# Performance work log

Measured on AMD Instinct MI355X. Metric: run time of the kernel, lower is better.

## Reference

```python
import jax, jax.numpy as jnp
import numpy as np

B = 8192        # number of contexts
T_SIDE = 10     # num_cx_tokens_per_side
NT = 10         # cx_max_num_types
V_TOK = 5000
V_TYP = 5000
D_TOK = 128
D_TYP = 32
H = 32          # hole_rnn_layer_size
D_IN = D_TOK + D_TYP  # 160


def setup_inputs() -> dict:
    key = jax.random.key(0)
    ks = jax.random.split(key, 32)
    def n(k, shape, scale=1.0):
        return jax.random.normal(k, shape, dtype=jnp.float32) * scale
    def rmask(k, shape):
        m = jax.random.randint(k, shape, 0, 2).astype(bool)
        return m.at[:, :, 0].set(True)  # first type slot always valid (as in data loader)
    inp = {}
    inp['tokens_before'] = jax.random.randint(ks[0], (B, T_SIDE), 0, V_TOK, dtype=jnp.int32)
    inp['types_before'] = jax.random.randint(ks[1], (B, T_SIDE, NT), 0, V_TYP, dtype=jnp.int32)
    inp['mask_before'] = rmask(ks[2], (B, T_SIDE, NT))
    inp['tokens_after'] = jax.random.randint(ks[3], (B, T_SIDE), 0, V_TOK, dtype=jnp.int32)
    inp['types_after'] = jax.random.randint(ks[4], (B, T_SIDE, NT), 0, V_TYP, dtype=jnp.int32)
    inp['mask_after'] = rmask(ks[5], (B, T_SIDE, NT))
    inp['token_embeddings'] = n(ks[6], (V_TOK, D_TOK))
    inp['type_embeddings'] = n(ks[7], (V_TYP, D_TYP))
    inp['hole_representation'] = n(ks[8], (1, 1, D_IN))
    # GRU kernels (TF GRUCell layout): gate kernel [(in+h), 2h], candidate [(in+h), h]
    i = 9
    for layer, din in ((0, D_IN), (1, 2 * H)):
        for d in ('fw', 'bw'):
            inp[f'gk_{d}{layer}'] = n(ks[i], (din + H, 2 * H), 0.1); i += 1
            inp[f'gb_{d}{layer}'] = jnp.zeros((2 * H,), jnp.float32)
            inp[f'ck_{d}{layer}'] = n(ks[i], (din + H, H), 0.1); i += 1
            inp[f'cb_{d}{layer}'] = jnp.zeros((H,), jnp.float32)
    return inp


def _embed(tokens, types, mask, tok_emb, typ_emb):
    te = tok_emb[tokens]                                 # [B,T,128]
    ty = typ_emb[types]                                  # [B,T,NT,32]
    ty = ty + (1.0 - mask[..., None].astype(jnp.float32)) * -1000.0
    ty = jnp.max(ty, axis=2)                             # masked max over types -> [B,T,32]
    return jnp.concatenate([te, ty], axis=-1)            # [B,T,160]


def _gru(x_seq, gk, gb, ck, cb):
    # x_seq: [T,B,D]; TF GRUCell math: r,u = sigmoid([x,h]Wg+bg); c = tanh([x, r*h]Wc+bc); h' = u*h+(1-u)*c
    h0 = jnp.zeros((x_seq.shape[1], cb.shape[0]), x_seq.dtype)
    def step(h, x):
        ru = jax.nn.sigmoid(jnp.concatenate([x, h], -1) @ gk + gb)
        r, u = jnp.split(ru, 2, axis=-1)
        c = jnp.tanh(jnp.concatenate([x, r * h], -1) @ ck + cb)
        h_new = u * h + (1.0 - u) * c
        return h_new, h_new
    _, ys = jax.lax.scan(step, h0, x_seq)
    return ys                                            # [T,B,H]


def _bidir(x_seq, pf, pb):
    fw = _gru(x_seq, *pf)
    bw = jnp.flip(_gru(jnp.flip(x_seq, 0), *pb), 0)
    return jnp.concatenate([fw, bw], axis=-1)            # [T,B,2H]


def reference(tokens_before, types_before, mask_before, tokens_after, types_after, mask_after,
              token_embeddings, type_embeddings, hole_representation,
              gk_fw0, gb_fw0, ck_fw0, cb_fw0, gk_bw0, gb_bw0, ck_bw0, cb_bw0,
              gk_fw1, gb_fw1, ck_fw1, cb_fw1, gk_bw1, gb_bw1, ck_bw1, cb_bw1):
    before = _embed(tokens_before, types_before, mask_before, token_embeddings, type_embeddings)
    after = _embed(tokens_after, types_after, mask_after, token_embeddings, type_embeddings)
    nb = before.shape[0]
    hole = jnp.broadcast_to(hole_representation, (nb, 1, D_IN))
    seq = jnp.concatenate([before, hole, after], axis=1)  # [B,21,160]
    x = jnp.transpose(seq, (1, 0, 2))                     # [T,B,D]
    y0 = _bidir(x, (gk_fw0, gb_fw0, ck_fw0, cb_fw0), (gk_bw0, gb_bw0, ck_bw0, cb_bw0))
    y1 = _bidir(y0, (gk_fw1, gb_fw1, ck_fw1, cb_fw1), (gk_bw1, gb_bw1, ck_bw1, cb_bw1))
    return jnp.transpose(y1, (1, 0, 2))                   # [B,21,64]
```

## Files before the change

kernel.cpp:

```cpp
#include <hip/hip_runtime.h>


typedef __attribute__((ext_vector_type(8))) short short8;
typedef __attribute__((ext_vector_type(8))) __bf16 bf16x8;
typedef __attribute__((ext_vector_type(4))) float f32x4;
typedef unsigned short ushort_t;

#define U_TOKEMB  0
#define U_TYPEMB  640000
#define U_HOLE    800000
#define U_GKFW0   800160
#define U_GBFW0   812448
#define U_CKFW0   812512
#define U_CBFW0   818656
#define U_GKBW0   818688
#define U_GBBW0   830976
#define U_CKBW0   831040
#define U_CBBW0   837184
#define U_GKFW1   837216
#define U_GBFW1   843360
#define U_CKFW1   843424
#define U_CBFW1   846496
#define U_GKBW1   846528
#define U_GBBW1   852672
#define U_CKBW1   852736
#define U_CBBW1   855808

#define MB_OFF    (2u << 20)
#define Y0A_OFF   (4u << 20)
#define TYPF_OFF  (25u << 20)

__device__ __forceinline__ float bf2f(unsigned int u) {
  union { unsigned int i; float f; } v; v.i = u << 16; return v.f;
}
__device__ __forceinline__ unsigned short f2bf(float f) {
  unsigned int u = __float_as_uint(f);
  u += 0x7fffu + ((u >> 16) & 1u);
  return (unsigned short)(u >> 16);
}
__device__ __forceinline__ f32x4 mfma16(short8 a, short8 b, f32x4 c) {
  return __builtin_amdgcn_mfma_f32_16x16x32_bf16(
      __builtin_bit_cast(bf16x8, a), __builtin_bit_cast(bf16x8, b), c, 0, 0, 0);
}
__device__ __forceinline__ float sgm(float x) {
  x = fminf(fmaxf(x, -30.f), 30.f);
  return 1.f / (1.f + __expf(-x));
}
__device__ __forceinline__ float tnh(float x) {
  x = fminf(fmaxf(x, -15.f), 15.f);
  float e = __expf(2.f * x);
  return (e - 1.f) / (e + 1.f);
}

__global__ void k0_detect(const ushort_t* __restrict__ probe_f,
                          const unsigned* __restrict__ probe_m,
                          const unsigned* __restrict__ probe_t,
                          int* __restrict__ flags) {
  const int lane = threadIdx.x;
  int cnt = 0;
#pragma unroll
  for (int i = 0; i < 4; ++i) {
    unsigned e = ((unsigned)probe_f[lane + i * 64] >> 7) & 0xffu;
    if (e == 0u || (e >= 112u && e <= 134u)) cnt++;
  }
#pragma unroll
  for (int off = 32; off > 0; off >>= 1) cnt += __shfl_down(cnt, off, 64);
  const unsigned v = probe_m[lane];
  const unsigned long long bytelike =
      __ballot((v > 1u) && (v != 0x3F800000u) && ((v & 0xFEFEFEFEu) == 0u));
  const unsigned tv = probe_t[lane];
  const unsigned long long tlooksTypes =
      __ballot(!(tv == 0u || tv == 1u || tv == 0x3F800000u));
  if (lane == 0) {
    flags[0] = (cnt < 205) ? 1 : 0;
    flags[1] = bytelike ? 1 : 0;
    flags[2] = tlooksTypes ? 0 : 1;
  }
}

struct Cvt19 { const void* src[19]; int len[19]; int dst[19]; };

__global__ void kcvt(Cvt19 a, ushort_t* __restrict__ cvt, const int* __restrict__ flags) {
  const int fp32 = flags[0];
  int gid = blockIdx.x * blockDim.x + threadIdx.x;
#pragma unroll 1
  for (int s = 0; s < 19; ++s) {
    if (gid < a.len[s]) {
      cvt[a.dst[s] + gid] = fp32 ? f2bf(((const float*)a.src[s])[gid])
                                 : ((const ushort_t*)a.src[s])[gid];
      return;
    }
    gid -= a.len[s];
  }
}

__global__ void kmask(const void* __restrict__ slot_tb, const void* __restrict__ slot_mb,
                      const void* __restrict__ slot_ta, const void* __restrict__ slot_ma,
                      ushort_t* __restrict__ mbits, const int* __restrict__ flags) {
  const int id = blockIdx.x * blockDim.x + threadIdx.x;
  if (id >= 163840) return;
  const int side = (id >= 81920) ? 1 : 0;
  const int idx = id - side * 81920;
  const int sw = flags[2];
  const void* src = side ? (sw ? slot_ta : slot_ma) : (sw ? slot_tb : slot_mb);
  unsigned bits = 0;
  if (flags[1] == 1) {
    const unsigned char* p = (const unsigned char*)src;
#pragma unroll
    for (int nt = 0; nt < 10; ++nt) bits |= (p[idx * 10 + nt] ? 1u : 0u) << nt;
  } else {
    const unsigned* p = (const unsigned*)src;
#pragma unroll
    for (int nt = 0; nt < 10; ++nt) bits |= (p[idx * 10 + nt] ? 1u : 0u) << nt;
  }
  mbits[side * 81920 + idx] = (ushort_t)bits;
}

__global__ __launch_bounds__(256) void ktypmax(
    const void* __restrict__ slot_tb, const void* __restrict__ slot_mb,
    const void* __restrict__ slot_ta, const void* __restrict__ slot_ma,
    const ushort_t* __restrict__ cvt, const ushort_t* __restrict__ mbits,
    uint4* __restrict__ typf, const int* __restrict__ flags) {
  const int wv = threadIdx.x >> 6;
  const int lane = threadIdx.x & 63;
  const int q = lane >> 4, nl = lane & 15;
  const int job = blockIdx.x * 4 + wv;
  const int st = job >> 9;
  const int btile = job & 511;
  const int side = (st >= 10) ? 1 : 0;
  const int ts = st - side * 10;
  const int b = btile * 16 + nl;
  const int sw = flags[2];
  const int* tys = side ? (const int*)(sw ? slot_ma : slot_ta)
                        : (const int*)(sw ? slot_mb : slot_tb);
  const unsigned bm = (unsigned)mbits[side * 81920 + b * 10 + ts];
  const int base = (b * 10 + ts) * 10;
  float mx[8];
#pragma unroll
  for (int j = 0; j < 8; ++j) mx[j] = -1e30f;
#pragma unroll
  for (int nt = 0; nt < 10; ++nt) {
    const int ty = tys[base + nt];
    const float pen = ((bm >> nt) & 1u) ? 0.f : -1000.f;
    uint4 e = *reinterpret_cast<const uint4*>(cvt + U_TYPEMB + (size_t)ty * 32 + q * 8);
    const unsigned w[4] = {e.x, e.y, e.z, e.w};
#pragma unroll
    for (int j2 = 0; j2 < 4; ++j2) {
      mx[2 * j2]     = fmaxf(mx[2 * j2],     bf2f(w[j2] & 0xffffu) + pen);
      mx[2 * j2 + 1] = fmaxf(mx[2 * j2 + 1], bf2f(w[j2] >> 16) + pen);
    }
  }
  short8 v;
#pragma unroll
  for (int j = 0; j < 8; ++j) v[j] = (short)f2bf(mx[j]);
  typf[(size_t)job * 64 + lane] = __builtin_bit_cast(uint4, v);
}

__device__ __forceinline__ void gatherX(
    int t, int btile, int lane,
    const int* __restrict__ tok_b, const int* __restrict__ tok_a,
    const ushort_t* __restrict__ cvt, const uint4* __restrict__ typf,
    short8 af[5]) {
  const int q = lane >> 4, nl = lane & 15;
  if (t == 10) {
#pragma unroll
    for (int kt = 0; kt < 5; ++kt)
      af[kt] = __builtin_bit_cast(short8,
          *reinterpret_cast<const uint4*>(cvt + U_HOLE + kt * 32 + q * 8));
    return;
  }
  const int ts = (t < 10) ? t : t - 11;
  const int side = (t < 10) ? 0 : 1;
  const int b = btile * 16 + nl;
  const int tok = (side ? tok_a : tok_b)[b * 10 + ts];
#pragma unroll
  for (int kt = 0; kt < 4; ++kt)
    af[kt] = __builtin_bit_cast(short8,
        *reinterpret_cast<const uint4*>(cvt + U_TOKEMB + (size_t)tok * 128 + kt * 32 + q * 8));
  af[4] = __builtin_bit_cast(short8,
      typf[((size_t)(side * 10 + ts) * 512 + btile) * 64 + lane]);
}

__global__ __launch_bounds__(256) void krec0(
    const int* __restrict__ tok_b, const int* __restrict__ tok_a,
    const ushort_t* __restrict__ cvt, const uint4* __restrict__ typf,
    uint4* __restrict__ y0a) {
  __shared__ __align__(16) ushort_t hbuf[4][2][16 * 40];
  const int wv = threadIdx.x >> 6;
  const int lane = threadIdx.x & 63;
  const int q = lane >> 4, nl = lane & 15;
  const int job = blockIdx.x * 4 + wv;
  const int dir = job & 1, btile = job >> 1;

  const ushort_t* gk = cvt + (dir ? U_GKBW0 : U_GKFW0);
  const ushort_t* ck = cvt + (dir ? U_CKBW0 : U_CKFW0);
  const ushort_t* gb = cvt + (dir ? U_GBBW0 : U_GBFW0);
  const ushort_t* cb = cvt + (dir ? U_CBBW0 : U_CBFW0);

  short8 wg[5][4], wc[5][2], wgh[4], wch[2];
#pragma unroll
  for (int kt = 0; kt < 5; ++kt) {
#pragma unroll
    for (int tn = 0; tn < 4; ++tn) {
      short8 v;
#pragma unroll
      for (int j = 0; j < 8; ++j) v[j] = (short)gk[(kt * 32 + q * 8 + j) * 64 + tn * 16 + nl];
      wg[kt][tn] = v;
    }
#pragma unroll
    for (int tn = 0; tn < 2; ++tn) {
      short8 v;
#pragma unroll
      for (int j = 0; j < 8; ++j) v[j] = (short)ck[(kt * 32 + q * 8 + j) * 32 + tn * 16 + nl];
      wc[kt][tn] = v;
    }
  }
#pragma unroll
  for (int tn = 0; tn < 4; ++tn) {
    short8 v;
#pragma unroll
    for (int j = 0; j < 8; ++j) v[j] = (short)gk[(160 + q * 8 + j) * 64 + tn * 16 + nl];
    wgh[tn] = v;
  }
#pragma unroll
  for (int tn = 0; tn < 2; ++tn) {
    short8 v;
#pragma unroll
    for (int j = 0; j < 8; ++j) v[j] = (short)ck[(160 + q * 8 + j) * 32 + tn * 16 + nl];
    wch[tn] = v;
  }
  float gb4[4], cb4[2];
#pragma unroll
  for (int tn = 0; tn < 4; ++tn) gb4[tn] = bf2f((unsigned)gb[tn * 16 + nl]);
#pragma unroll
  for (int tn = 0; tn < 2; ++tn) cb4[tn] = bf2f((unsigned)cb[tn * 16 + nl]);

  f32x4 hc0 = {0.f, 0.f, 0.f, 0.f}, hc1 = {0.f, 0.f, 0.f, 0.f};
  short8 hA = {0, 0, 0, 0, 0, 0, 0, 0};
  ushort_t* hb0 = hbuf[wv][0];
  ushort_t* hb1 = hbuf[wv][1];

  short8 afc[5], afn[5];
  gatherX(dir ? 20 : 0, btile, lane, tok_b, tok_a, cvt, typf, afc);

  for (int s = 0; s < 21; ++s) {
    const int t = dir ? 20 - s : s;
    if (s < 20)
      gatherX(dir ? t - 1 : t + 1, btile, lane, tok_b, tok_a, cvt, typf, afn);

    f32x4 ru[4];
#pragma unroll
    for (int tn = 0; tn < 4; ++tn) {
      f32x4 acc = {gb4[tn], gb4[tn], gb4[tn], gb4[tn]};
#pragma unroll
      for (int kt = 0; kt < 5; ++kt) acc = mfma16(afc[kt], wg[kt][tn], acc);
      acc = mfma16(hA, wgh[tn], acc);
      ru[tn] = acc;
    }
#pragma unroll
    for (int tn = 0; tn < 4; ++tn)
#pragma unroll
      for (int r = 0; r < 4; ++r) ru[tn][r] = sgm(ru[tn][r]);

#pragma unroll
    for (int r = 0; r < 4; ++r) {
      hb0[(q * 4 + r) * 40 + nl]      = f2bf(ru[0][r] * hc0[r]);
      hb0[(q * 4 + r) * 40 + 16 + nl] = f2bf(ru[1][r] * hc1[r]);
    }
    short8 rhA = *reinterpret_cast<const short8*>(hb0 + nl * 40 + q * 8);

    f32x4 cc0 = {cb4[0], cb4[0], cb4[0], cb4[0]};
    f32x4 cc1 = {cb4[1], cb4[1], cb4[1], cb4[1]};
#pragma unroll
    for (int kt = 0; kt < 5; ++kt) {
      cc0 = mfma16(afc[kt], wc[kt][0], cc0);
      cc1 = mfma16(afc[kt], wc[kt][1], cc1);
    }
    cc0 = mfma16(rhA, wch[0], cc0);
    cc1 = mfma16(rhA, wch[1], cc1);
#pragma unroll
    for (int r = 0; r < 4; ++r) {
      const float c0 = tnh(cc0[r]), c1 = tnh(cc1[r]);
      const float u0 = ru[2][r], u1 = ru[3][r];
      hc0[r] = u0 * hc0[r] + (1.f - u0) * c0;
      hc1[r] = u1 * hc1[r] + (1.f - u1) * c1;
    }

#pragma unroll
    for (int r = 0; r < 4; ++r) {
      hb1[(q * 4 + r) * 40 + nl]      = f2bf(hc0[r]);
      hb1[(q * 4 + r) * 40 + 16 + nl] = f2bf(hc1[r]);
    }
    hA = *reinterpret_cast<const short8*>(hb1 + nl * 40 + q * 8);
    y0a[((size_t)(t * 512 + btile) * 2 + dir) * 64 + lane] = __builtin_bit_cast(uint4, hA);

    if (s < 20) {
#pragma unroll
      for (int kt = 0; kt < 5; ++kt) afc[kt] = afn[kt];
    }
  }
}

__global__ __launch_bounds__(256) void k3b(
    const ushort_t* __restrict__ cvt, const uint4* __restrict__ y0a,
    float* __restrict__ out) {
  __shared__ __align__(16) ushort_t hbuf[4][2][16 * 40];
  const int wv = threadIdx.x >> 6;
  const int lane = threadIdx.x & 63;
  const int q = lane >> 4, nl = lane & 15;
  const int job = blockIdx.x * 4 + wv;
  const int dir = job & 1, btile = job >> 1;
  const ushort_t* gk = cvt + (dir ? U_GKBW1 : U_GKFW1);
  const ushort_t* ck = cvt + (dir ? U_CKBW1 : U_CKFW1);
  const ushort_t* gb = cvt + (dir ? U_GBBW1 : U_GBFW1);
  const ushort_t* cb = cvt + (dir ? U_CBBW1 : U_CBFW1);

  short8 wg[3][4], wc[3][2];
#pragma unroll
  for (int kt = 0; kt < 3; ++kt) {
#pragma unroll
    for (int tn = 0; tn < 4; ++tn) {
      short8 v;
#pragma unroll
      for (int j = 0; j < 8; ++j) v[j] = (short)gk[(kt * 32 + q * 8 + j) * 64 + tn * 16 + nl];
      wg[kt][tn] = v;
    }
#pragma unroll
    for (int tn = 0; tn < 2; ++tn) {
      short8 v;
#pragma unroll
      for (int j = 0; j < 8; ++j) v[j] = (short)ck[(kt * 32 + q * 8 + j) * 32 + tn * 16 + nl];
      wc[kt][tn] = v;
    }
  }
  float gb4[4], cb4[2];
#pragma unroll
  for (int tn = 0; tn < 4; ++tn) gb4[tn] = bf2f((unsigned)gb[tn * 16 + nl]);
#pragma unroll
  for (int tn = 0; tn < 2; ++tn) cb4[tn] = bf2f((unsigned)cb[tn * 16 + nl]);

  f32x4 hc0 = {0.f, 0.f, 0.f, 0.f}, hc1 = {0.f, 0.f, 0.f, 0.f};
  short8 hA = {0, 0, 0, 0, 0, 0, 0, 0};
  ushort_t* hb0 = hbuf[wv][0];
  ushort_t* hb1 = hbuf[wv][1];

  short8 ya0, ya1, yn0, yn1;
  {
    const int t0 = dir ? 20 : 0;
    ya0 = __builtin_bit_cast(short8, y0a[((size_t)(t0 * 512 + btile) * 2 + 0) * 64 + lane]);
    ya1 = __builtin_bit_cast(short8, y0a[((size_t)(t0 * 512 + btile) * 2 + 1) * 64 + lane]);
  }

  for (int s = 0; s < 21; ++s) {
    const int t = dir ? 20 - s : s;
    if (s < 20) {
      const int t2 = dir ? t - 1 : t + 1;
      yn0 = __builtin_bit_cast(short8, y0a[((size_t)(t2 * 512 + btile) * 2 + 0) * 64 + lane]);
      yn1 = __builtin_bit_cast(short8, y0a[((size_t)(t2 * 512 + btile) * 2 + 1) * 64 + lane]);
    }

    f32x4 ru[4];
#pragma unroll
    for (int tn = 0; tn < 4; ++tn) {
      f32x4 acc = {gb4[tn], gb4[tn], gb4[tn], gb4[tn]};
      acc = mfma16(ya0, wg[0][tn], acc);
      acc = mfma16(ya1, wg[1][tn], acc);
      acc = mfma16(hA,  wg[2][tn], acc);
      ru[tn] = acc;
    }
#pragma unroll
    for (int tn = 0; tn < 4; ++tn)
#pragma unroll
      for (int r = 0; r < 4; ++r) ru[tn][r] = sgm(ru[tn][r]);

#pragma unroll
    for (int r = 0; r < 4; ++r) {
      hb0[(q * 4 + r) * 40 + nl]      = f2bf(ru[0][r] * hc0[r]);
      hb0[(q * 4 + r) * 40 + 16 + nl] = f2bf(ru[1][r] * hc1[r]);
    }
    short8 rhA = *reinterpret_cast<const short8*>(hb0 + nl * 40 + q * 8);

    f32x4 cc0 = {cb4[0], cb4[0], cb4[0], cb4[0]};
    cc0 = mfma16(ya0, wc[0][0], cc0);
    cc0 = mfma16(ya1, wc[1][0], cc0);
    cc0 = mfma16(rhA, wc[2][0], cc0);
    f32x4 cc1 = {cb4[1], cb4[1], cb4[1], cb4[1]};
    cc1 = mfma16(ya0, wc[0][1], cc1);
    cc1 = mfma16(ya1, wc[1][1], cc1);
    cc1 = mfma16(rhA, wc[2][1], cc1);

#pragma unroll
    for (int r = 0; r < 4; ++r) {
      const float c0 = tnh(cc0[r]), c1 = tnh(cc1[r]);
      const float u0 = ru[2][r], u1 = ru[3][r];
      hc0[r] = u0 * hc0[r] + (1.f - u0) * c0;
      hc1[r] = u1 * hc1[r] + (1.f - u1) * c1;
    }

#pragma unroll
    for (int r = 0; r < 4; ++r) {
      hb1[(q * 4 + r) * 40 + nl]      = f2bf(hc0[r]);
      hb1[(q * 4 + r) * 40 + 16 + nl] = f2bf(hc1[r]);
    }
    hA = *reinterpret_cast<const short8*>(hb1 + nl * 40 + q * 8);

#pragma unroll
    for (int r = 0; r < 4; ++r) {
      const size_t o = ((size_t)(btile * 16 + q * 4 + r) * 21 + t) * 64 + dir * 32 + nl;
      out[o]      = hc0[r];
      out[o + 16] = hc1[r];
    }

    if (s < 20) { ya0 = yn0; ya1 = yn1; }
  }
}

extern "C" void kernel_launch(void* const* d_in, const int* in_sizes, int n_in,
                              void* d_out, int out_size, void* d_ws, size_t ws_size,
                              hipStream_t stream)
{
  const int* tok_b = (const int*)d_in[0];
  const void* slot_tb = d_in[1];
  const void* slot_mb = d_in[2];
  const int* tok_a = (const int*)d_in[3];
  const void* slot_ta = d_in[4];
  const void* slot_ma = d_in[5];

  int* flags = (int*)d_ws;
  ushort_t* cvt = (ushort_t*)((char*)d_ws + 64);
  ushort_t* mbits = (ushort_t*)((char*)d_ws + MB_OFF);
  uint4* y0a = (uint4*)((char*)d_ws + Y0A_OFF);
  uint4* typf = (uint4*)((char*)d_ws + TYPF_OFF);

  k0_detect<<<dim3(1), dim3(64), 0, stream>>>(
      (const ushort_t*)d_in[6], (const unsigned*)slot_mb, (const unsigned*)slot_tb,
      flags);

  static const int slen[19] = {640000, 160000, 160,
                               12288, 64, 6144, 32, 12288, 64, 6144, 32,
                               6144, 64, 3072, 32, 6144, 64, 3072, 32};
  static const int sdst[19] = {U_TOKEMB, U_TYPEMB, U_HOLE,
                               U_GKFW0, U_GBFW0, U_CKFW0, U_CBFW0,
                               U_GKBW0, U_GBBW0, U_CKBW0, U_CBBW0,
                               U_GKFW1, U_GBFW1, U_CKFW1, U_CBFW1,
                               U_GKBW1, U_GBBW1, U_CKBW1, U_CBBW1};
  Cvt19 a;
  int tot = 0;
  for (int i = 0; i < 19; ++i) {
    a.src[i] = d_in[6 + i]; a.len[i] = slen[i]; a.dst[i] = sdst[i]; tot += slen[i];
  }
  kcvt<<<dim3((tot + 255) / 256), dim3(256), 0, stream>>>(a, cvt, flags);

  kmask<<<dim3(640), dim3(256), 0, stream>>>(
      slot_tb, slot_mb, slot_ta, slot_ma, mbits, flags);

  ktypmax<<<dim3(2560), dim3(256), 0, stream>>>(
      slot_tb, slot_mb, slot_ta, slot_ma, cvt, mbits, typf, flags);

  krec0<<<dim3(256), dim3(256), 0, stream>>>(tok_b, tok_a, cvt, typf, y0a);

  k3b<<<dim3(256), dim3(256), 0, stream>>>(cvt, y0a, (float*)d_out);
}
```

Before: 205.1 us.

## Split GRU hidden columns across two waves and fold mask packing into typmax

The recurrent kernels now put each (batch tile, direction) job on a two-wave block, with each wave computing half of the hidden columns. The waves exchange r*h and h through shared memory with __syncthreads, which quadruples the block count and shortens the per-step MFMA chain. The separate mask-bitpacking kernel is removed and ktypmax reads the mask directly, saving one launch and a round trip through memory. Sigmoid and tanh use fast reciprocal division, and the extra barriers add per-step sync cost.

Result: slower. 229.9 us (+12.1%).

```diff
diff --git a/kernel.cpp b/kernel.cpp
--- a/kernel.cpp
+++ b/kernel.cpp
@@ -26,7 +26,6 @@
 #define U_CKBW1   852736
 #define U_CBBW1   855808
 
-#define MB_OFF    (2u << 20)
 #define Y0A_OFF   (4u << 20)
 #define TYPF_OFF  (25u << 20)
 
@@ -44,12 +43,12 @@
 }
 __device__ __forceinline__ float sgm(float x) {
   x = fminf(fmaxf(x, -30.f), 30.f);
-  return 1.f / (1.f + __expf(-x));
+  return __fdividef(1.f, 1.f + __expf(-x));
 }
 __device__ __forceinline__ float tnh(float x) {
   x = fminf(fmaxf(x, -15.f), 15.f);
   float e = __expf(2.f * x);
-  return (e - 1.f) / (e + 1.f);
+  return (e - 1.f) * __fdividef(1.f, e + 1.f);
 }
 
 __global__ void k0_detect(const ushort_t* __restrict__ probe_f,
@@ -94,33 +93,11 @@
   }
 }
 
-__global__ void kmask(const void* __restrict__ slot_tb, const void* __restrict__ slot_mb,
-                      const void* __restrict__ slot_ta, const void* __restrict__ slot_ma,
-                      ushort_t* __restrict__ mbits, const int* __restrict__ flags) {
-  const int id = blockIdx.x * blockDim.x + threadIdx.x;
-  if (id >= 163840) return;
-  const int side = (id >= 81920) ? 1 : 0;
-  const int idx = id - side * 81920;
-  const int sw = flags[2];
-  const void* src = side ? (sw ? slot_ta : slot_ma) : (sw ? slot_tb : slot_mb);
-  unsigned bits = 0;
-  if (flags[1] == 1) {
-    const unsigned char* p = (const unsigned char*)src;
-#pragma unroll
-    for (int nt = 0; nt < 10; ++nt) bits |= (p[idx * 10 + nt] ? 1u : 0u) << nt;
-  } else {
-    const unsigned* p = (const unsigned*)src;
-#pragma unroll
-    for (int nt = 0; nt < 10; ++nt) bits |= (p[idx * 10 + nt] ? 1u : 0u) << nt;
-  }
-  mbits[side * 81920 + idx] = (ushort_t)bits;
-}
-
 __global__ __launch_bounds__(256) void ktypmax(
     const void* __restrict__ slot_tb, const void* __restrict__ slot_mb,
     const void* __restrict__ slot_ta, const void* __restrict__ slot_ma,
-    const ushort_t* __restrict__ cvt, const ushort_t* __restrict__ mbits,
-    uint4* __restrict__ typf, const int* __restrict__ flags) {
+    const ushort_t* __restrict__ cvt, uint4* __restrict__ typf,
+    const int* __restrict__ flags) {
   const int wv = threadIdx.x >> 6;
   const int lane = threadIdx.x & 63;
   const int q = lane >> 4, nl = lane & 15;
@@ -131,9 +108,11 @@
   const int ts = st - side * 10;
   const int b = btile * 16 + nl;
   const int sw = flags[2];
+  const int bytem = flags[1];
   const int* tys = side ? (const int*)(sw ? slot_ma : slot_ta)
                         : (const int*)(sw ? slot_mb : slot_tb);
-  const unsigned bm = (unsigned)mbits[side * 81920 + b * 10 + ts];
+  const void* msk = side ? (sw ? slot_ta : slot_ma)
+                         : (sw ? slot_tb : slot_mb);
   const int base = (b * 10 + ts) * 10;
   float mx[8];
 #pragma unroll
@@ -141,7 +120,9 @@
 #pragma unroll
   for (int nt = 0; nt < 10; ++nt) {
     const int ty = tys[base + nt];
-    const float pen = ((bm >> nt) & 1u) ? 0.f : -1000.f;
+    const bool mv = bytem ? (((const unsigned char*)msk)[base + nt] != 0)
+                          : (((const unsigned*)msk)[base + nt] != 0u);
+    const float pen = mv ? 0.f : -1000.f;
     uint4 e = *reinterpret_cast<const uint4*>(cvt + U_TYPEMB + (size_t)ty * 32 + q * 8);
     const unsigned w[4] = {e.x, e.y, e.z, e.w};
 #pragma unroll
@@ -181,15 +162,16 @@
       typf[((size_t)(side * 10 + ts) * 512 + btile) * 64 + lane]);
 }
 
-__global__ __launch_bounds__(256) void krec0(
+__global__ __launch_bounds__(128) void krec0(
     const int* __restrict__ tok_b, const int* __restrict__ tok_a,
     const ushort_t* __restrict__ cvt, const uint4* __restrict__ typf,
     uint4* __restrict__ y0a) {
-  __shared__ __align__(16) ushort_t hbuf[4][2][16 * 40];
-  const int wv = threadIdx.x >> 6;
+  __shared__ __align__(16) ushort_t hb0[16 * 40];
+  __shared__ __align__(16) ushort_t hb1[16 * 40];
+  const int w = threadIdx.x >> 6;
   const int lane = threadIdx.x & 63;
   const int q = lane >> 4, nl = lane & 15;
-  const int job = blockIdx.x * 4 + wv;
+  const int job = blockIdx.x;
   const int dir = job & 1, btile = job >> 1;
 
   const ushort_t* gk = cvt + (dir ? U_GKBW0 : U_GKFW0);
@@ -197,48 +179,36 @@
   const ushort_t* gb = cvt + (dir ? U_GBBW0 : U_GBFW0);
   const ushort_t* cb = cvt + (dir ? U_CBBW0 : U_CBFW0);
 
-  short8 wg[5][4], wc[5][2], wgh[4], wch[2];
+  short8 wgr[5], wgu[5], wcn[5], wghr, wghu, wchn;
 #pragma unroll
   for (int kt = 0; kt < 5; ++kt) {
-#pragma unroll
-    for (int tn = 0; tn < 4; ++tn) {
-      short8 v;
-#pragma unroll
-      for (int j = 0; j < 8; ++j) v[j] = (short)gk[(kt * 32 + q * 8 + j) * 64 + tn * 16 + nl];
-      wg[kt][tn] = v;
-    }
-#pragma unroll
-    for (int tn = 0; tn < 2; ++tn) {
-      short8 v;
-#pragma unroll
-      for (int j = 0; j < 8; ++j) v[j] = (short)ck[(kt * 32 + q * 8 + j) * 32 + tn * 16 + nl];
-      wc[kt][tn] = v;
-    }
-  }
-#pragma unroll
-  for (int tn = 0; tn < 4; ++tn) {
-    short8 v;
-#pragma unroll
-    for (int j = 0; j < 8; ++j) v[j] = (short)gk[(160 + q * 8 + j) * 64 + tn * 16 + nl];
-    wgh[tn] = v;
-  }
-#pragma unroll
-  for (int tn = 0; tn < 2; ++tn) {
-    short8 v;
-#pragma unroll
-    for (int j = 0; j < 8; ++j) v[j] = (short)ck[(160 + q * 8 + j) * 32 + tn * 16 + nl];
-    wch[tn] = v;
-  }
-  float gb4[4], cb4[2];
-#pragma unroll
-  for (int tn = 0; tn < 4; ++tn) gb4[tn] = bf2f((unsigned)gb[tn * 16 + nl]);
-#pragma unroll
-  for (int tn = 0; tn < 2; ++tn) cb4[tn] = bf2f((unsigned)cb[tn * 16 + nl]);
-
-  f32x4 hc0 = {0.f, 0.f, 0.f, 0.f}, hc1 = {0.f, 0.f, 0.f, 0.f};
+    short8 vr, vu, vc;
+#pragma unroll
+    for (int j = 0; j < 8; ++j) {
+      const int row = kt * 32 + q * 8 + j;
+      vr[j] = (short)gk[row * 64 + w * 16 + nl];
+      vu[j] = (short)gk[row * 64 + (2 + w) * 16 + nl];
+      vc[j] = (short)ck[row * 32 + w * 16 + nl];
+    }
+    wgr[kt] = vr; wgu[kt] = vu; wcn[kt] = vc;
+  }
+  {
+    short8 vr, vu, vc;
+#pragma unroll
+    for (int j = 0; j < 8; ++j) {
+      const int row = 160 + q * 8 + j;
+      vr[j] = (short)gk[row * 64 + w * 16 + nl];
+      vu[j] = (short)gk[row * 64 + (2 + w) * 16 + nl];
+      vc[j] = (short)ck[row * 32 + w * 16 + nl];
+    }
+    wghr = vr; wghu = vu; wchn = vc;
+  }
+  const float gbr = bf2f((unsigned)gb[w * 16 + nl]);
+  const float gbu = bf2f((unsigned)gb[(2 + w) * 16 + nl]);
+  const float cbn = bf2f((unsigned)cb[w * 16 + nl]);
+
+  f32x4 hc = {0.f, 0.f, 0.f, 0.f};
   short8 hA = {0, 0, 0, 0, 0, 0, 0, 0};
-  ushort_t* hb0 = hbuf[wv][0];
-  ushort_t* hb1 = hbuf[wv][1];
 
   short8 afc[5], afn[5];
   gatherX(dir ? 20 : 0, btile, lane, tok_b, tok_a, cvt, typf, afc);
@@ -248,51 +218,41 @@
     if (s < 20)
       gatherX(dir ? t - 1 : t + 1, btile, lane, tok_b, tok_a, cvt, typf, afn);
 
-    f32x4 ru[4];
-#pragma unroll
-    for (int tn = 0; tn < 4; ++tn) {
-      f32x4 acc = {gb4[tn], gb4[tn], gb4[tn], gb4[tn]};
-#pragma unroll
-      for (int kt = 0; kt < 5; ++kt) acc = mfma16(afc[kt], wg[kt][tn], acc);
-      acc = mfma16(hA, wgh[tn], acc);
-      ru[tn] = acc;
-    }
-#pragma unroll
-    for (int tn = 0; tn < 4; ++tn)
-#pragma unroll
-      for (int r = 0; r < 4; ++r) ru[tn][r] = sgm(ru[tn][r]);
-
+    f32x4 rr = {gbr, gbr, gbr, gbr};
+    f32x4 uu = {gbu, gbu, gbu, gbu};
+#pragma unroll
+    for (int kt = 0; kt < 5; ++kt) {
+      rr = mfma16(afc[kt], wgr[kt], rr);
+      uu = mfma16(afc[kt], wgu[kt], uu);
+    }
+    rr = mfma16(hA, wghr, rr);
+    uu = mfma16(hA, wghu, uu);
+#pragma unroll
+    for (int r = 0; r < 4; ++r) { rr[r] = sgm(rr[r]); uu[r] = sgm(uu[r]); }
+
+#pragma unroll
+    for (int r = 0; r < 4; ++r)
+      hb0[(q * 4 + r) * 40 + w * 16 + nl] = f2bf(rr[r] * hc[r]);
+    __syncthreads();
+    short8 rhA = *reinterpret_cast<const short8*>(hb0 + nl * 40 + q * 8);
+
+    f32x4 cc = {cbn, cbn, cbn, cbn};
+#pragma unroll
+    for (int kt = 0; kt < 5; ++kt) cc = mfma16(afc[kt], wcn[kt], cc);
+    cc = mfma16(rhA, wchn, cc);
 #pragma unroll
     for (int r = 0; r < 4; ++r) {
-      hb0[(q * 4 + r) * 40 + nl]      = f2bf(ru[0][r] * hc0[r]);
-      hb0[(q * 4 + r) * 40 + 16 + nl] = f2bf(ru[1][r] * hc1[r]);
-    }
-    short8 rhA = *reinterpret_cast<const short8*>(hb0 + nl * 40 + q * 8);
-
-    f32x4 cc0 = {cb4[0], cb4[0], cb4[0], cb4[0]};
-    f32x4 cc1 = {cb4[1], cb4[1], cb4[1], cb4[1]};
-#pragma unroll
-    for (int kt = 0; kt < 5; ++kt) {
-      cc0 = mfma16(afc[kt], wc[kt][0], cc0);
-      cc1 = mfma16(afc[kt], wc[kt][1], cc1);
-    }
-    cc0 = mfma16(rhA, wch[0], cc0);
-    cc1 = mfma16(rhA, wch[1], cc1);
-#pragma unroll
-    for (int r = 0; r < 4; ++r) {
-      const float c0 = tnh(cc0[r]), c1 = tnh(cc1[r]);
-      const float u0 = ru[2][r], u1 = ru[3][r];
-      hc0[r] = u0 * hc0[r] + (1.f - u0) * c0;
-      hc1[r] = u1 * hc1[r] + (1.f - u1) * c1;
-    }
-
-#pragma unroll
-    for (int r = 0; r < 4; ++r) {
-      hb1[(q * 4 + r) * 40 + nl]      = f2bf(hc0[r]);
-      hb1[(q * 4 + r) * 40 + 16 + nl] = f2bf(hc1[r]);
-    }
+      const float c = tnh(cc[r]);
+      hc[r] = uu[r] * hc[r] + (1.f - uu[r]) * c;
+    }
+
+#pragma unroll
+    for (int r = 0; r < 4; ++r)
+      hb1[(q * 4 + r) * 40 + w * 16 + nl] = f2bf(hc[r]);
+    __syncthreads();
     hA = *reinterpret_cast<const short8*>(hb1 + nl * 40 + q * 8);
-    y0a[((size_t)(t * 512 + btile) * 2 + dir) * 64 + lane] = __builtin_bit_cast(uint4, hA);
+    if (w == 0)
+      y0a[((size_t)(t * 512 + btile) * 2 + dir) * 64 + lane] = __builtin_bit_cast(uint4, hA);
 
     if (s < 20) {
 #pragma unroll
@@ -301,48 +261,40 @@
   }
 }
 
-__global__ __launch_bounds__(256) void k3b(
+__global__ __launch_bounds__(128) void k3b(
     const ushort_t* __restrict__ cvt, const uint4* __restrict__ y0a,
     float* __restrict__ out) {
-  __shared__ __align__(16) ushort_t hbuf[4][2][16 * 40];
-  const int wv = threadIdx.x >> 6;
+  __shared__ __align__(16) ushort_t hb0[16 * 40];
+  __shared__ __align__(16) ushort_t hb1[16 * 40];
+  const int w = threadIdx.x >> 6;
   const int lane = threadIdx.x & 63;
   const int q = lane >> 4, nl = lane & 15;
-  const int job = blockIdx.x * 4 + wv;
+  const int job = blockIdx.x;
   const int dir = job & 1, btile = job >> 1;
   const ushort_t* gk = cvt + (dir ? U_GKBW1 : U_GKFW1);
   const ushort_t* ck = cvt + (dir ? U_CKBW1 : U_CKFW1);
   const ushort_t* gb = cvt + (dir ? U_GBBW1 : U_GBFW1);
   const ushort_t* cb = cvt + (dir ? U_CBBW1 : U_CBFW1);
 
-  short8 wg[3][4], wc[3][2];
+  short8 wgr[3], wgu[3], wcn[3];
 #pragma unroll
   for (int kt = 0; kt < 3; ++kt) {
-#pragma unroll
-    for (int tn = 0; tn < 4; ++tn) {
-      short8 v;
-#pragma unroll
-      for (int j = 0; j < 8; ++j) v[j] = (short)gk[(kt * 32 + q * 8 + j) * 64 + tn * 16 + nl];
-      wg[kt][tn] = v;
-    }
-#pragma unroll
-    for (int tn = 0; tn < 2; ++tn) {
-      short8 v;
-#pragma unroll
-      for (int j = 0; j < 8; ++j) v[j] = (short)ck[(kt * 32 + q * 8 + j) * 32 + tn * 16 + nl];
-      wc[kt][tn] = v;
-    }
-  }
-  float gb4[4], cb4[2];
-#pragma unroll
-  for (int tn = 0; tn < 4; ++tn) gb4[tn] = bf2f((unsigned)gb[tn * 16 + nl]);
-#pragma unroll
-  for (int tn = 0; tn < 2; ++tn) cb4[tn] = bf2f((unsigned)cb[tn * 16 + nl]);
-
-  f32x4 hc0 = {0.f, 0.f, 0.f, 0.f}, hc1 = {0.f, 0.f, 0.f, 0.f};
+    short8 vr, vu, vc;
+#pragma unroll
+    for (int j = 0; j < 8; ++j) {
+      const int row = kt * 32 + q * 8 + j;
+      vr[j] = (short)gk[row * 64 + w * 16 + nl];
+      vu[j] = (short)gk[row * 64 + (2 + w) * 16 + nl];
+      vc[j] = (short)ck[row * 32 + w * 16 + nl];
+    }
+    wgr[kt] = vr; wgu[kt] = vu; wcn[kt] = vc;
+  }
+  const float gbr = bf2f((unsigned)gb[w * 16 + nl]);
+  const float gbu = bf2f((unsigned)gb[(2 + w) * 16 + nl]);
+  const float cbn = bf2f((unsigned)cb[w * 16 + nl]);
+
+  f32x4 hc = {0.f, 0.f, 0.f, 0.f};
   short8 hA = {0, 0, 0, 0, 0, 0, 0, 0};
-  ushort_t* hb0 = hbuf[wv][0];
-  ushort_t* hb1 = hbuf[wv][1];
 
   short8 ya0, ya1, yn0, yn1;
   {
@@ -359,56 +311,43 @@
       yn1 = __builtin_bit_cast(short8, y0a[((size_t)(t2 * 512 + btile) * 2 + 1) * 64 + lane]);
     }
 
-    f32x4 ru[4];
-#pragma unroll
-    for (int tn = 0; tn < 4; ++tn) {
-      f32x4 acc = {gb4[tn], gb4[tn], gb4[tn], gb4[tn]};
-      acc = mfma16(ya0, wg[0][tn], acc);
-      acc = mfma16(ya1, wg[1][tn], acc);
-      acc = mfma16(hA,  wg[2][tn], acc);
-      ru[tn] = acc;
-    }
-#pragma unroll
-    for (int tn = 0; tn < 4; ++tn)
-#pragma unroll
-      for (int r = 0; r < 4; ++r) ru[tn][r] = sgm(ru[tn][r]);
-
+    f32x4 rr = {gbr, gbr, gbr, gbr};
+    f32x4 uu = {gbu, gbu, gbu, gbu};
+    rr = mfma16(ya0, wgr[0], rr);
+    uu = mfma16(ya0, wgu[0], uu);
+    rr = mfma16(ya1, wgr[1], rr);
+    uu = mfma16(ya1, wgu[1], uu);
+    rr = mfma16(hA, wgr[2], rr);
+    uu = mfma16(hA, wgu[2], uu);
+#pragma unroll
+    for (int r = 0; r < 4; ++r) { rr[r] = sgm(rr[r]); uu[r] = sgm(uu[r]); }
+
+#pragma unroll
+    for (int r = 0; r < 4; ++r)
+      hb0[(q * 4 + r) * 40 + w * 16 + nl] = f2bf(rr[r] * hc[r]);
+    __syncthreads();
+    short8 rhA = *reinterpret_cast<const short8*>(hb0 + nl * 40 + q * 8);
+
+    f32x4 cc = {cbn, cbn, cbn, cbn};
+    cc = mfma16(ya0, wcn[0], cc);
+    cc = mfma16(ya1, wcn[1], cc);
+    cc = mfma16(rhA, wcn[2], cc);
 #pragma unroll
     for (int r = 0; r < 4; ++r) {
-      hb0[(q * 4 + r) * 40 + nl]      = f2bf(ru[0][r] * hc0[r]);
-      hb0[(q * 4 + r) * 40 + 16 + nl] = f2bf(ru[1][r] * hc1[r]);
-    }
-    short8 rhA = *reinterpret_cast<const short8*>(hb0 + nl * 40 + q * 8);
-
-    f32x4 cc0 = {cb4[0], cb4[0], cb4[0], cb4[0]};
-    cc0 = mfma16(ya0, wc[0][0], cc0);
-    cc0 = mfma16(ya1, wc[1][0], cc0);
-    cc0 = mfma16(rhA, wc[2][0], cc0);
-    f32x4 cc1 = {cb4[1], cb4[1], cb4[1], cb4[1]};
-    cc1 = mfma16(ya0, wc[0][1], cc1);
-    cc1 = mfma16(ya1, wc[1][1], cc1);
-    cc1 = mfma16(rhA, wc[2][1], cc1);
+      const float c = tnh(cc[r]);
+      hc[r] = uu[r] * hc[r] + (1.f - uu[r]) * c;
+    }
+
+#pragma unroll
+    for (int r = 0; r < 4; ++r)
+      hb1[(q * 4 + r) * 40 + w * 16 + nl] = f2bf(hc[r]);
+    __syncthreads();
+    hA = *reinterpret_cast<const short8*>(hb1 + nl * 40 + q * 8);
 
 #pragma unroll
     for (int r = 0; r < 4; ++r) {
-      const float c0 = tnh(cc0[r]), c1 = tnh(cc1[r]);
-      const float u0 = ru[2][r], u1 = ru[3][r];
-      hc0[r] = u0 * hc0[r] + (1.f - u0) * c0;
-      hc1[r] = u1 * hc1[r] + (1.f - u1) * c1;
-    }
-
-#pragma unroll
-    for (int r = 0; r < 4; ++r) {
-      hb1[(q * 4 + r) * 40 + nl]      = f2bf(hc0[r]);
-      hb1[(q * 4 + r) * 40 + 16 + nl] = f2bf(hc1[r]);
-    }
-    hA = *reinterpret_cast<const short8*>(hb1 + nl * 40 + q * 8);
-
-#pragma unroll
-    for (int r = 0; r < 4; ++r) {
-      const size_t o = ((size_t)(btile * 16 + q * 4 + r) * 21 + t) * 64 + dir * 32 + nl;
-      out[o]      = hc0[r];
-      out[o + 16] = hc1[r];
+      const size_t o = ((size_t)(btile * 16 + q * 4 + r) * 21 + t) * 64 + dir * 32 + w * 16 + nl;
+      out[o] = hc[r];
     }
 
     if (s < 20) { ya0 = yn0; ya1 = yn1; }
@@ -428,7 +367,6 @@
 
   int* flags = (int*)d_ws;
   ushort_t* cvt = (ushort_t*)((char*)d_ws + 64);
-  ushort_t* mbits = (ushort_t*)((char*)d_ws + MB_OFF);
   uint4* y0a = (uint4*)((char*)d_ws + Y0A_OFF);
   uint4* typf = (uint4*)((char*)d_ws + TYPF_OFF);
 
@@ -451,13 +389,10 @@
   }
   kcvt<<<dim3((tot + 255) / 256), dim3(256), 0, stream>>>(a, cvt, flags);
 
-  kmask<<<dim3(640), dim3(256), 0, stream>>>(
-      slot_tb, slot_mb, slot_ta, slot_ma, mbits, flags);
-
   ktypmax<<<dim3(2560), dim3(256), 0, stream>>>(
-      slot_tb, slot_mb, slot_ta, slot_ma, cvt, mbits, typf, flags);
-
-  krec0<<<dim3(256), dim3(256), 0, stream>>>(tok_b, tok_a, cvt, typf, y0a);
-
-  k3b<<<dim3(256), dim3(256), 0, stream>>>(cvt, y0a, (float*)d_out);
-}
+      slot_tb, slot_mb, slot_ta, slot_ma, cvt, typf, flags);
+
+  krec0<<<dim3(1024), dim3(128), 0, stream>>>(tok_b, tok_a, cvt, typf, y0a);
+
+  k3b<<<dim3(1024), dim3(128), 0, stream>>>(cvt, y0a, (float*)d_out);
+}
```

## Fold mask-bit kernel into type max-pool and use fast divides

Applied to the files above, without the earlier changes.

Removes the separate kmask kernel and reads the mask bytes or words directly inside ktypmax, which drops one launch and the intermediate mbits buffer. The sigmoid and tanh helpers switch to __fdividef for cheaper, less precise division. krec0 and k3b get a min-blocks-per-CU launch bound of 1, which lets the compiler use more registers per thread. Fast division changes the rounding of the gate activations slightly.

Result: slower. 212.3 us (+3.5%).

```diff
diff --git a/kernel.cpp b/kernel.cpp
--- a/kernel.cpp
+++ b/kernel.cpp
@@ -26,7 +26,6 @@
 #define U_CKBW1   852736
 #define U_CBBW1   855808
 
-#define MB_OFF    (2u << 20)
 #define Y0A_OFF   (4u << 20)
 #define TYPF_OFF  (25u << 20)
 
@@ -44,12 +43,12 @@
 }
 __device__ __forceinline__ float sgm(float x) {
   x = fminf(fmaxf(x, -30.f), 30.f);
-  return 1.f / (1.f + __expf(-x));
+  return __fdividef(1.f, 1.f + __expf(-x));
 }
 __device__ __forceinline__ float tnh(float x) {
   x = fminf(fmaxf(x, -15.f), 15.f);
   float e = __expf(2.f * x);
-  return (e - 1.f) / (e + 1.f);
+  return (e - 1.f) * __fdividef(1.f, e + 1.f);
 }
 
 __global__ void k0_detect(const ushort_t* __restrict__ probe_f,
@@ -94,33 +93,11 @@
   }
 }
 
-__global__ void kmask(const void* __restrict__ slot_tb, const void* __restrict__ slot_mb,
-                      const void* __restrict__ slot_ta, const void* __restrict__ slot_ma,
-                      ushort_t* __restrict__ mbits, const int* __restrict__ flags) {
-  const int id = blockIdx.x * blockDim.x + threadIdx.x;
-  if (id >= 163840) return;
-  const int side = (id >= 81920) ? 1 : 0;
-  const int idx = id - side * 81920;
-  const int sw = flags[2];
-  const void* src = side ? (sw ? slot_ta : slot_ma) : (sw ? slot_tb : slot_mb);
-  unsigned bits = 0;
-  if (flags[1] == 1) {
-    const unsigned char* p = (const unsigned char*)src;
-#pragma unroll
-    for (int nt = 0; nt < 10; ++nt) bits |= (p[idx * 10 + nt] ? 1u : 0u) << nt;
-  } else {
-    const unsigned* p = (const unsigned*)src;
-#pragma unroll
-    for (int nt = 0; nt < 10; ++nt) bits |= (p[idx * 10 + nt] ? 1u : 0u) << nt;
-  }
-  mbits[side * 81920 + idx] = (ushort_t)bits;
-}
-
 __global__ __launch_bounds__(256) void ktypmax(
     const void* __restrict__ slot_tb, const void* __restrict__ slot_mb,
     const void* __restrict__ slot_ta, const void* __restrict__ slot_ma,
-    const ushort_t* __restrict__ cvt, const ushort_t* __restrict__ mbits,
-    uint4* __restrict__ typf, const int* __restrict__ flags) {
+    const ushort_t* __restrict__ cvt, uint4* __restrict__ typf,
+    const int* __restrict__ flags) {
   const int wv = threadIdx.x >> 6;
   const int lane = threadIdx.x & 63;
   const int q = lane >> 4, nl = lane & 15;
@@ -131,9 +108,11 @@
   const int ts = st - side * 10;
   const int b = btile * 16 + nl;
   const int sw = flags[2];
+  const int bytem = flags[1];
   const int* tys = side ? (const int*)(sw ? slot_ma : slot_ta)
                         : (const int*)(sw ? slot_mb : slot_tb);
-  const unsigned bm = (unsigned)mbits[side * 81920 + b * 10 + ts];
+  const void* msk = side ? (sw ? slot_ta : slot_ma)
+                         : (sw ? slot_tb : slot_mb);
   const int base = (b * 10 + ts) * 10;
   float mx[8];
 #pragma unroll
@@ -141,7 +120,9 @@
 #pragma unroll
   for (int nt = 0; nt < 10; ++nt) {
     const int ty = tys[base + nt];
-    const float pen = ((bm >> nt) & 1u) ? 0.f : -1000.f;
+    const bool mv = bytem ? (((const unsigned char*)msk)[base + nt] != 0)
+                          : (((const unsigned*)msk)[base + nt] != 0u);
+    const float pen = mv ? 0.f : -1000.f;
     uint4 e = *reinterpret_cast<const uint4*>(cvt + U_TYPEMB + (size_t)ty * 32 + q * 8);
     const unsigned w[4] = {e.x, e.y, e.z, e.w};
 #pragma unroll
@@ -181,7 +162,7 @@
       typf[((size_t)(side * 10 + ts) * 512 + btile) * 64 + lane]);
 }
 
-__global__ __launch_bounds__(256) void krec0(
+__global__ __launch_bounds__(256, 1) void krec0(
     const int* __restrict__ tok_b, const int* __restrict__ tok_a,
     const ushort_t* __restrict__ cvt, const uint4* __restrict__ typf,
     uint4* __restrict__ y0a) {
@@ -301,7 +282,7 @@
   }
 }
 
-__global__ __launch_bounds__(256) void k3b(
+__global__ __launch_bounds__(256, 1) void k3b(
     const ushort_t* __restrict__ cvt, const uint4* __restrict__ y0a,
     float* __restrict__ out) {
   __shared__ __align__(16) ushort_t hbuf[4][2][16 * 40];
@@ -428,7 +409,6 @@
 
   int* flags = (int*)d_ws;
   ushort_t* cvt = (ushort_t*)((char*)d_ws + 64);
-  ushort_t* mbits = (ushort_t*)((char*)d_ws + MB_OFF);
   uint4* y0a = (uint4*)((char*)d_ws + Y0A_OFF);
   uint4* typf = (uint4*)((char*)d_ws + TYPF_OFF);
 
@@ -451,11 +431,8 @@
   }
   kcvt<<<dim3((tot + 255) / 256), dim3(256), 0, stream>>>(a, cvt, flags);
 
-  kmask<<<dim3(640), dim3(256), 0, stream>>>(
-      slot_tb, slot_mb, slot_ta, slot_ma, mbits, flags);
-
   ktypmax<<<dim3(2560), dim3(256), 0, stream>>>(
-      slot_tb, slot_mb, slot_ta, slot_ma, cvt, mbits, typf, flags);
+      slot_tb, slot_mb, slot_ta, slot_ma, cvt, typf, flags);
 
   krec0<<<dim3(256), dim3(256), 0, stream>>>(tok_b, tok_a, cvt, typf, y0a);
 
```
